# Performance work log

Measured on AMD Instinct MI355X. Metric: run time of the kernel, lower is better.

## Reference

```python
import jax, jax.numpy as jnp
import numpy as np

SIGMA = 0.2
BN_EPS = 1e-5


def setup_inputs() -> dict:
    key = jax.random.key(0)
    k1, k2, k3, k4 = jax.random.split(key, 4)
    B, F, K, M = 8, 16384, 3, 64
    normals = jax.random.normal(k1, (B, 3, F), dtype=jnp.float32)
    # normalize to unit vectors (face normals), keeps math well-conditioned
    normals = normals / jnp.linalg.norm(normals, axis=1, keepdims=True)
    weight_alpha = jax.random.uniform(k2, (1, M, 4), dtype=jnp.float32) * np.pi
    weight_beta = jax.random.uniform(k3, (1, M, 4), dtype=jnp.float32) * 2 * np.pi
    bn_gamma = jnp.ones((M,), dtype=jnp.float32)
    bn_beta = jnp.zeros((M,), dtype=jnp.float32)
    neighbor_index = jax.random.randint(k4, (B, F, K), 0, F, dtype=jnp.int64)
    return {"normals": normals, "weight_alpha": weight_alpha,
            "weight_beta": weight_beta, "bn_gamma": bn_gamma,
            "bn_beta": bn_beta, "neighbor_index": neighbor_index}


def reference(normals, weight_alpha, weight_beta, bn_gamma, bn_beta, neighbor_index):
    # normals: [B, 3, F]; neighbor_index: [B, F, K]
    B, _, F = normals.shape
    K = neighbor_index.shape[-1]
    # kernel points on unit sphere from spherical angles: [3, M, 4]
    sa, ca = jnp.sin(weight_alpha), jnp.cos(weight_alpha)
    sb, cb = jnp.sin(weight_beta), jnp.cos(weight_beta)
    w = jnp.concatenate([sa * cb, sa * sb, ca], axis=0)  # [3, M, 4]

    nt = jnp.transpose(normals, (0, 2, 1))  # [B, F, 3]
    # gather neighbor normals per batch: [B, F, K, 3]
    neigh = jax.vmap(lambda n, idx: n[idx])(nt, neighbor_index)
    # points per face: center + K neighbors -> [B, F, K+1, 3]
    pts = jnp.concatenate([nt[:, :, None, :], neigh], axis=2)

    # squared distance via expansion: ||p||^2 + ||w||^2 - 2 p.w
    dot = jnp.einsum('bfic,cmj->bmfij', pts, w)        # [B, M, F, K+1, 4]
    p2 = jnp.sum(pts * pts, axis=-1)                   # [B, F, K+1]
    w2 = jnp.sum(w * w, axis=0)                        # [M, 4]
    dist = (p2[:, None, :, :, None] + w2[None, :, None, None, :] - 2.0 * dot)

    feat = jnp.sum(jnp.exp(dist / (-2.0 * SIGMA ** 2)), axis=(3, 4))
    feat = feat / float((K + 1) * 4)                   # [B, M, F]

    # BatchNorm1d (training-mode batch stats over B and F per channel M)
    mean = jnp.mean(feat, axis=(0, 2), keepdims=True)
    var = jnp.var(feat, axis=(0, 2), keepdims=True)
    xhat = (feat - mean) / jnp.sqrt(var + BN_EPS)
    out = xhat * bn_gamma[None, :, None] + bn_beta[None, :, None]
    return jax.nn.relu(out)
```

## Files before the change

kernel.cpp:

```cpp
#include <hip/hip_runtime.h>

#define B_DIM 8
#define F_DIM 16384
#define K_DIM 3
#define M_DIM 64
#define MCH   16
#define LOG2E 1.4426950408889634f

#define WS_Q 32768

__global__ __launch_bounds__(256) void fkc_feat_kernel(
    const float* __restrict__ normals,
    const float* __restrict__ walpha,
    const float* __restrict__ wbeta,
    const int*   __restrict__ nidx,
    float* __restrict__ feat_out,
    float* __restrict__ ws)
{
    __shared__ float4 sW[MCH * 4];
    __shared__ float sRS[MCH][32];
    __shared__ float sRQ[MCH][32];

    const int tid = threadIdx.x;
    const int b  = blockIdx.x >> 8;
    const int mc = (blockIdx.x >> 6) & 3;
    const int fc = blockIdx.x & 63;

    if (tid < MCH * 4) {
        int idx = mc * MCH * 4 + tid;
        float a = walpha[idx], bb = wbeta[idx];
        float sa = sinf(a), ca = cosf(a);
        float sb = sinf(bb), cb = cosf(bb);
        float wx = sa * cb, wy = sa * sb, wz = ca;
        float w2 = wx * wx + wy * wy + wz * wz;
        sW[tid] = make_float4(wx * 25.0f * LOG2E, wy * 25.0f * LOG2E,
                              wz * 25.0f * LOG2E, -12.5f * LOG2E * (w2 + 1.0f));
    }
    __syncthreads();

    const int f = (fc << 8) + tid;
    const float* nb = normals + (size_t)b * 3 * F_DIM;
    float px[4], py[4], pz[4];
    px[0] = nb[f]; py[0] = nb[F_DIM + f]; pz[0] = nb[2 * F_DIM + f];
    const int* ib = nidx + ((size_t)b * F_DIM + f) * K_DIM;
#pragma unroll
    for (int k = 0; k < K_DIM; ++k) {
        int id = ib[k];
        px[k + 1] = nb[id]; py[k + 1] = nb[F_DIM + id]; pz[k + 1] = nb[2 * F_DIM + id];
    }

    const int wave = tid >> 6, lane = tid & 63;
    float* outb = feat_out + ((size_t)b * M_DIM + mc * MCH) * F_DIM + f;
#pragma unroll 2
    for (int m = 0; m < MCH; ++m) {
        float s0 = 0.f, s1 = 0.f, s2 = 0.f, s3 = 0.f;
#pragma unroll
        for (int j = 0; j < 4; ++j) {
            float4 w = sW[m * 4 + j];
            s0 += __builtin_amdgcn_exp2f(fmaf(w.x, px[0], fmaf(w.y, py[0], fmaf(w.z, pz[0], w.w))));
            s1 += __builtin_amdgcn_exp2f(fmaf(w.x, px[1], fmaf(w.y, py[1], fmaf(w.z, pz[1], w.w))));
            s2 += __builtin_amdgcn_exp2f(fmaf(w.x, px[2], fmaf(w.y, py[2], fmaf(w.z, pz[2], w.w))));
            s3 += __builtin_amdgcn_exp2f(fmaf(w.x, px[3], fmaf(w.y, py[3], fmaf(w.z, pz[3], w.w))));
        }
        float fv = ((s0 + s1) + (s2 + s3)) * (1.0f / 16.0f);
        outb[(size_t)m * F_DIM] = fv;

        float s = fv, q = fv * fv;
        s += __shfl_xor(s, 8, 64);  q += __shfl_xor(q, 8, 64);
        s += __shfl_xor(s, 16, 64); q += __shfl_xor(q, 16, 64);
        s += __shfl_xor(s, 32, 64); q += __shfl_xor(q, 32, 64);
        if (lane < 8) { sRS[m][wave * 8 + lane] = s; sRQ[m][wave * 8 + lane] = q; }
    }
    __syncthreads();

    {
        const int m = tid >> 4, j = tid & 15;
        float s = sRS[m][j] + sRS[m][j + 16];
        float q = sRQ[m][j] + sRQ[m][j + 16];
        s += __shfl_xor(s, 1, 64);  q += __shfl_xor(q, 1, 64);
        s += __shfl_xor(s, 2, 64);  q += __shfl_xor(q, 2, 64);
        s += __shfl_xor(s, 4, 64);  q += __shfl_xor(q, 4, 64);
        s += __shfl_xor(s, 8, 64);  q += __shfl_xor(q, 8, 64);
        if (j == 0) {
            int slot = (mc * MCH + m) * 512 + b * 64 + fc;
            ws[slot] = s;
            ws[WS_Q + slot] = q;
        }
    }
}

__global__ __launch_bounds__(256) void fkc_bn_kernel(
    float* __restrict__ out,
    const float* __restrict__ gamma,
    const float* __restrict__ beta,
    const float* __restrict__ ws)
{
    __shared__ float sS[4], sQ[4];
    __shared__ float sAC[2];
    const int row = blockIdx.x;
    const int m = row & 63;
    const int tid = threadIdx.x;
    const int wave = tid >> 6, lane = tid & 63;

    {
        float s = ws[m * 512 + tid]         + ws[m * 512 + tid + 256];
        float q = ws[WS_Q + m * 512 + tid]  + ws[WS_Q + m * 512 + tid + 256];
#pragma unroll
        for (int off = 32; off >= 1; off >>= 1) {
            s += __shfl_xor(s, off, 64);
            q += __shfl_xor(q, off, 64);
        }
        if (lane == 0) { sS[wave] = s; sQ[wave] = q; }
    }
    __syncthreads();
    if (tid == 0) {
        float s = (sS[0] + sS[1]) + (sS[2] + sS[3]);
        float q = (sQ[0] + sQ[1]) + (sQ[2] + sQ[3]);
        const float invcnt = 1.0f / (float)(B_DIM * F_DIM);
        float mean = s * invcnt;
        float var  = q * invcnt - mean * mean;
        float inv  = rsqrtf(var + 1e-5f);
        float A = gamma[m] * inv;
        sAC[0] = A;
        sAC[1] = beta[m] - mean * A;
    }
    __syncthreads();

    const float A = sAC[0], C = sAC[1];
    float4* p4 = (float4*)(out + (size_t)row * F_DIM);
#pragma unroll
    for (int i = 0; i < 16; ++i) {
        float4 v = p4[tid + i * 256];
        v.x = fmaxf(fmaf(v.x, A, C), 0.0f);
        v.y = fmaxf(fmaf(v.y, A, C), 0.0f);
        v.z = fmaxf(fmaf(v.z, A, C), 0.0f);
        v.w = fmaxf(fmaf(v.w, A, C), 0.0f);
        p4[tid + i * 256] = v;
    }
}

extern "C" void kernel_launch(void* const* d_in, const int* in_sizes, int n_in,
                              void* d_out, int out_size, void* d_ws, size_t ws_size,
                              hipStream_t stream)
{
    const float* normals = (const float*)d_in[0];
    const float* walpha  = (const float*)d_in[1];
    const float* wbeta   = (const float*)d_in[2];
    const float* gamma   = (const float*)d_in[3];
    const float* beta    = (const float*)d_in[4];
    const int*   nidx    = (const int*)d_in[5];
    float* out = (float*)d_out;
    float* ws  = (float*)d_ws;

    hipLaunchKernelGGL(fkc_feat_kernel, dim3(2048), dim3(256), 0, stream,
                       normals, walpha, wbeta, nidx, out, ws);
    hipLaunchKernelGGL(fkc_bn_kernel, dim3(B_DIM * M_DIM), dim3(256), 0, stream,
                       out, gamma, beta, ws);
}
```

Before: 50.85 us.

## Precompute per-face kernel responses once, then gather and sum neighbor rows

The feature is a sum over points of per-point Gaussian responses, and each face's response is reused as a neighbor of other faces. The new code first computes a table G[b,f,m] once per face, then a gather kernel sums the center row and three neighbor rows, writes the features and computes partial BN statistics through a shared-memory transpose. This cuts exp evaluations roughly fourfold but adds a 32 MB workspace write and random 256-byte row gathers. The old path is kept as a fallback for when the workspace is too small.

```diff
diff --git a/kernel.cpp b/kernel.cpp
--- a/kernel.cpp
+++ b/kernel.cpp
@@ -4,30 +4,206 @@
 #define F_DIM 16384
 #define K_DIM 3
 #define M_DIM 64
-#define MCH   16
 #define LOG2E 1.4426950408889634f
 
-#define WS_Q 32768
-
-__global__ __launch_bounds__(256) void fkc_feat_kernel(
+#define WS_Q   65536
+#define WS_G   131072
+#define WS_NEED ((size_t)(WS_G + (size_t)B_DIM * F_DIM * M_DIM) * sizeof(float))
+
+#define FB_WS_Q 32768
+
+__global__ __launch_bounds__(256) void fkc_g_kernel(
     const float* __restrict__ normals,
     const float* __restrict__ walpha,
     const float* __restrict__ wbeta,
+    float* __restrict__ G)
+{
+    __shared__ float4 sW[256];
+    const int tid = threadIdx.x;
+    {
+        float a = walpha[tid], b = wbeta[tid];
+        float sa = sinf(a), ca = cosf(a);
+        float sb = sinf(b), cb = cosf(b);
+        float wx = sa * cb, wy = sa * sb, wz = ca;
+        float w2 = wx * wx + wy * wy + wz * wz;
+        sW[tid] = make_float4(wx * 25.0f * LOG2E, wy * 25.0f * LOG2E,
+                              wz * 25.0f * LOG2E, -12.5f * LOG2E * (w2 + 1.0f));
+    }
+    __syncthreads();
+
+    const int b  = blockIdx.x >> 8;
+    const int fc = blockIdx.x & 255;
+    const int fl = tid & 63, mq = tid >> 6;
+    const int f  = (fc << 6) + fl;
+
+    const float* nb = normals + (size_t)b * 3 * F_DIM;
+    const float px = nb[f], py = nb[F_DIM + f], pz = nb[2 * F_DIM + f];
+
+    float4* gp = (float4*)(G + ((size_t)(b * F_DIM + f)) * M_DIM + mq * 16);
+#pragma unroll
+    for (int r = 0; r < 4; ++r) {
+        float v[4];
+#pragma unroll
+        for (int c = 0; c < 4; ++c) {
+            const int m = mq * 16 + r * 4 + c;
+            float4 w0 = sW[m * 4 + 0], w1 = sW[m * 4 + 1];
+            float4 w2 = sW[m * 4 + 2], w3 = sW[m * 4 + 3];
+            float e0 = __builtin_amdgcn_exp2f(fmaf(w0.x, px, fmaf(w0.y, py, fmaf(w0.z, pz, w0.w))));
+            float e1 = __builtin_amdgcn_exp2f(fmaf(w1.x, px, fmaf(w1.y, py, fmaf(w1.z, pz, w1.w))));
+            float e2 = __builtin_amdgcn_exp2f(fmaf(w2.x, px, fmaf(w2.y, py, fmaf(w2.z, pz, w2.w))));
+            float e3 = __builtin_amdgcn_exp2f(fmaf(w3.x, px, fmaf(w3.y, py, fmaf(w3.z, pz, w3.w))));
+            v[c] = (e0 + e1) + (e2 + e3);
+        }
+        gp[r] = make_float4(v[0], v[1], v[2], v[3]);
+    }
+}
+
+__global__ __launch_bounds__(256) void fkc_gather_kernel(
+    const float* __restrict__ G,
     const int*   __restrict__ nidx,
-    float* __restrict__ feat_out,
+    float* __restrict__ out,
     float* __restrict__ ws)
 {
-    __shared__ float4 sW[MCH * 4];
-    __shared__ float sRS[MCH][32];
-    __shared__ float sRQ[MCH][32];
-
+    __shared__ float T[2][128][34];
+    const int tid = threadIdx.x;
+    const int b  = blockIdx.x >> 7;
+    const int fc = blockIdx.x & 127;
+    const int fl = tid & 127, mh = tid >> 7;
+    const int f  = (fc << 7) + fl;
+
+    const int* ib = nidx + ((size_t)(b * F_DIM + f)) * K_DIM;
+    const int i1 = ib[0], i2 = ib[1], i3 = ib[2];
+
+    const size_t gb = (size_t)b * F_DIM * M_DIM + (size_t)mh * 32;
+    const float4* r0 = (const float4*)(G + gb + (size_t)f  * M_DIM);
+    const float4* r1 = (const float4*)(G + gb + (size_t)i1 * M_DIM);
+    const float4* r2 = (const float4*)(G + gb + (size_t)i2 * M_DIM);
+    const float4* r3 = (const float4*)(G + gb + (size_t)i3 * M_DIM);
+
+    float4 acc[8];
+#pragma unroll
+    for (int r = 0; r < 8; ++r) {
+        float4 a = r0[r], c = r1[r], d = r2[r], e = r3[r];
+        acc[r] = make_float4((a.x + c.x) + (d.x + e.x), (a.y + c.y) + (d.y + e.y),
+                             (a.z + c.z) + (d.z + e.z), (a.w + c.w) + (d.w + e.w));
+    }
+
+    {
+        float* ob = out + ((size_t)b * M_DIM + mh * 32) * F_DIM + f;
+#pragma unroll
+        for (int r = 0; r < 8; ++r) {
+            ob[(size_t)(r * 4 + 0) * F_DIM] = acc[r].x;
+            ob[(size_t)(r * 4 + 1) * F_DIM] = acc[r].y;
+            ob[(size_t)(r * 4 + 2) * F_DIM] = acc[r].z;
+            ob[(size_t)(r * 4 + 3) * F_DIM] = acc[r].w;
+        }
+    }
+
+    const int rmh = tid >> 7, rml = (tid >> 2) & 31, rfs = tid & 3;
+    float ps;
+#pragma unroll
+    for (int r = 0; r < 8; ++r) {
+        *(float2*)&T[mh][fl][r * 4 + 0] = make_float2(acc[r].x, acc[r].y);
+        *(float2*)&T[mh][fl][r * 4 + 2] = make_float2(acc[r].z, acc[r].w);
+    }
+    __syncthreads();
+    {
+        float s = 0.f;
+#pragma unroll
+        for (int i = 0; i < 32; ++i) s += T[rmh][rfs * 32 + i][rml];
+        s += __shfl_xor(s, 1, 64);
+        s += __shfl_xor(s, 2, 64);
+        ps = s;
+    }
+    __syncthreads();
+#pragma unroll
+    for (int r = 0; r < 8; ++r) {
+        *(float2*)&T[mh][fl][r * 4 + 0] = make_float2(acc[r].x * acc[r].x, acc[r].y * acc[r].y);
+        *(float2*)&T[mh][fl][r * 4 + 2] = make_float2(acc[r].z * acc[r].z, acc[r].w * acc[r].w);
+    }
+    __syncthreads();
+    {
+        float q = 0.f;
+#pragma unroll
+        for (int i = 0; i < 32; ++i) q += T[rmh][rfs * 32 + i][rml];
+        q += __shfl_xor(q, 1, 64);
+        q += __shfl_xor(q, 2, 64);
+        if (rfs == 0) {
+            int m = rmh * 32 + rml;
+            int slot = m * 1024 + b * 128 + fc;
+            ws[slot] = ps;
+            ws[WS_Q + slot] = q;
+        }
+    }
+}
+
+__global__ __launch_bounds__(256) void fkc_bn2_kernel(
+    float* __restrict__ out,
+    const float* __restrict__ gamma,
+    const float* __restrict__ beta,
+    const float* __restrict__ ws)
+{
+    __shared__ float sS[4], sQ[4];
+    __shared__ float sAC[2];
+    const int row = blockIdx.x;
+    const int m = row & 63;
+    const int tid = threadIdx.x;
+    const int wave = tid >> 6, lane = tid & 63;
+
+    {
+        const float* p = ws + m * 1024;
+        const float* r = ws + WS_Q + m * 1024;
+        float s = (p[tid] + p[tid + 256]) + (p[tid + 512] + p[tid + 768]);
+        float q = (r[tid] + r[tid + 256]) + (r[tid + 512] + r[tid + 768]);
+#pragma unroll
+        for (int off = 32; off >= 1; off >>= 1) {
+            s += __shfl_xor(s, off, 64);
+            q += __shfl_xor(q, off, 64);
+        }
+        if (lane == 0) { sS[wave] = s; sQ[wave] = q; }
+    }
+    __syncthreads();
+    if (tid == 0) {
+        float s = (sS[0] + sS[1]) + (sS[2] + sS[3]);
+        float q = (sQ[0] + sQ[1]) + (sQ[2] + sQ[3]);
+        const float invcnt = 1.0f / (float)(B_DIM * F_DIM);
+        float meanS = s * invcnt;
+        float meanF = meanS * (1.0f / 16.0f);
+        float ef2   = q * invcnt * (1.0f / 256.0f);
+        float var   = ef2 - meanF * meanF;
+        float inv   = rsqrtf(var + 1e-5f);
+        float A = gamma[m] * inv;
+        sAC[0] = A * (1.0f / 16.0f);
+        sAC[1] = beta[m] - meanF * A;
+    }
+    __syncthreads();
+
+    const float A = sAC[0], C = sAC[1];
+    float4* p4 = (float4*)(out + (size_t)row * F_DIM);
+#pragma unroll
+    for (int i = 0; i < 16; ++i) {
+        float4 v = p4[tid + i * 256];
+        v.x = fmaxf(fmaf(v.x, A, C), 0.0f);
+        v.y = fmaxf(fmaf(v.y, A, C), 0.0f);
+        v.z = fmaxf(fmaf(v.z, A, C), 0.0f);
+        v.w = fmaxf(fmaf(v.w, A, C), 0.0f);
+        p4[tid + i * 256] = v;
+    }
+}
+
+__global__ __launch_bounds__(256) void fb_feat_kernel(
+    const float* __restrict__ normals, const float* __restrict__ walpha,
+    const float* __restrict__ wbeta, const int* __restrict__ nidx,
+    float* __restrict__ feat_out, float* __restrict__ ws)
+{
+    __shared__ float4 sW[64];
+    __shared__ float sRS[16][32], sRQ[16][32];
     const int tid = threadIdx.x;
     const int b  = blockIdx.x >> 8;
     const int mc = (blockIdx.x >> 6) & 3;
     const int fc = blockIdx.x & 63;
-
-    if (tid < MCH * 4) {
-        int idx = mc * MCH * 4 + tid;
+    if (tid < 64) {
+        int idx = mc * 64 + tid;
         float a = walpha[idx], bb = wbeta[idx];
         float sa = sinf(a), ca = cosf(a);
         float sb = sinf(bb), cb = cosf(bb);
@@ -37,7 +213,6 @@
                               wz * 25.0f * LOG2E, -12.5f * LOG2E * (w2 + 1.0f));
     }
     __syncthreads();
-
     const int f = (fc << 8) + tid;
     const float* nb = normals + (size_t)b * 3 * F_DIM;
     float px[4], py[4], pz[4];
@@ -48,11 +223,10 @@
         int id = ib[k];
         px[k + 1] = nb[id]; py[k + 1] = nb[F_DIM + id]; pz[k + 1] = nb[2 * F_DIM + id];
     }
-
     const int wave = tid >> 6, lane = tid & 63;
-    float* outb = feat_out + ((size_t)b * M_DIM + mc * MCH) * F_DIM + f;
+    float* outb = feat_out + ((size_t)b * M_DIM + mc * 16) * F_DIM + f;
 #pragma unroll 2
-    for (int m = 0; m < MCH; ++m) {
+    for (int m = 0; m < 16; ++m) {
         float s0 = 0.f, s1 = 0.f, s2 = 0.f, s3 = 0.f;
 #pragma unroll
         for (int j = 0; j < 4; ++j) {
@@ -64,7 +238,6 @@
         }
         float fv = ((s0 + s1) + (s2 + s3)) * (1.0f / 16.0f);
         outb[(size_t)m * F_DIM] = fv;
-
         float s = fv, q = fv * fv;
         s += __shfl_xor(s, 8, 64);  q += __shfl_xor(q, 8, 64);
         s += __shfl_xor(s, 16, 64); q += __shfl_xor(q, 16, 64);
@@ -72,7 +245,6 @@
         if (lane < 8) { sRS[m][wave * 8 + lane] = s; sRQ[m][wave * 8 + lane] = q; }
     }
     __syncthreads();
-
     {
         const int m = tid >> 4, j = tid & 15;
         float s = sRS[m][j] + sRS[m][j + 16];
@@ -82,18 +254,16 @@
         s += __shfl_xor(s, 4, 64);  q += __shfl_xor(q, 4, 64);
         s += __shfl_xor(s, 8, 64);  q += __shfl_xor(q, 8, 64);
         if (j == 0) {
-            int slot = (mc * MCH + m) * 512 + b * 64 + fc;
+            int slot = (mc * 16 + m) * 512 + b * 64 + fc;
             ws[slot] = s;
-            ws[WS_Q + slot] = q;
-        }
-    }
-}
-
-__global__ __launch_bounds__(256) void fkc_bn_kernel(
-    float* __restrict__ out,
-    const float* __restrict__ gamma,
-    const float* __restrict__ beta,
-    const float* __restrict__ ws)
+            ws[FB_WS_Q + slot] = q;
+        }
+    }
+}
+
+__global__ __launch_bounds__(256) void fb_bn_kernel(
+    float* __restrict__ out, const float* __restrict__ gamma,
+    const float* __restrict__ beta, const float* __restrict__ ws)
 {
     __shared__ float sS[4], sQ[4];
     __shared__ float sAC[2];
@@ -101,10 +271,9 @@
     const int m = row & 63;
     const int tid = threadIdx.x;
     const int wave = tid >> 6, lane = tid & 63;
-
-    {
-        float s = ws[m * 512 + tid]         + ws[m * 512 + tid + 256];
-        float q = ws[WS_Q + m * 512 + tid]  + ws[WS_Q + m * 512 + tid + 256];
+    {
+        float s = ws[m * 512 + tid]           + ws[m * 512 + tid + 256];
+        float q = ws[FB_WS_Q + m * 512 + tid] + ws[FB_WS_Q + m * 512 + tid + 256];
 #pragma unroll
         for (int off = 32; off >= 1; off >>= 1) {
             s += __shfl_xor(s, off, 64);
@@ -125,7 +294,6 @@
         sAC[1] = beta[m] - mean * A;
     }
     __syncthreads();
-
     const float A = sAC[0], C = sAC[1];
     float4* p4 = (float4*)(out + (size_t)row * F_DIM);
 #pragma unroll
@@ -152,8 +320,17 @@
     float* out = (float*)d_out;
     float* ws  = (float*)d_ws;
 
-    hipLaunchKernelGGL(fkc_feat_kernel, dim3(2048), dim3(256), 0, stream,
-                       normals, walpha, wbeta, nidx, out, ws);
-    hipLaunchKernelGGL(fkc_bn_kernel, dim3(B_DIM * M_DIM), dim3(256), 0, stream,
-                       out, gamma, beta, ws);
-}
+    if (ws_size >= WS_NEED) {
+        hipLaunchKernelGGL(fkc_g_kernel, dim3(2048), dim3(256), 0, stream,
+                           normals, walpha, wbeta, ws + WS_G);
+        hipLaunchKernelGGL(fkc_gather_kernel, dim3(1024), dim3(256), 0, stream,
+                           ws + WS_G, nidx, out, ws);
+        hipLaunchKernelGGL(fkc_bn2_kernel, dim3(B_DIM * M_DIM), dim3(256), 0, stream,
+                           out, gamma, beta, ws);
+    } else {
+        hipLaunchKernelGGL(fb_feat_kernel, dim3(2048), dim3(256), 0, stream,
+                           normals, walpha, wbeta, nidx, out, ws);
+        hipLaunchKernelGGL(fb_bn_kernel, dim3(B_DIM * M_DIM), dim3(256), 0, stream,
+                           out, gamma, beta, ws);
+    }
+}
```

Measured after the change: 71.33 us. 40.3% more time.
